# Performance work log

Measured on AMD Instinct MI355X. Metric: run time of the kernel, lower is better.

Reference implementation:

```python
import jax, jax.numpy as jnp
import numpy as np

HIDDEN = 1024
NUM_HEADS = 16
HEAD_DIM = HIDDEN // NUM_HEADS
WINDOW = 64
B, S = 2, 4096


def setup_inputs() -> dict:
    key = jax.random.key(0)
    ks = jax.random.split(key, 8)
    d = {
        'query': jax.random.normal(ks[0], (B, S, HIDDEN), jnp.float32),
        'key':   jax.random.normal(ks[1], (B, S, HIDDEN), jnp.float32),
        'value': jax.random.normal(ks[2], (B, S, HIDDEN), jnp.float32),
        'Wq': jax.random.normal(ks[3], (HIDDEN, HIDDEN), jnp.float32) * 0.02,
        'bq': jnp.zeros((HIDDEN,), jnp.float32),
        'Wk': jax.random.normal(ks[4], (HIDDEN, HIDDEN), jnp.float32) * 0.02,
        'bk': jnp.zeros((HIDDEN,), jnp.float32),
        'Wv': jax.random.normal(ks[5], (HIDDEN, HIDDEN), jnp.float32) * 0.02,
        'bv': jnp.zeros((HIDDEN,), jnp.float32),
        'Wo': jax.random.normal(ks[6], (HIDDEN, HIDDEN), jnp.float32) * 0.02,
        'bo': jnp.zeros((HIDDEN,), jnp.float32),
    }
    return d


def reference(query, key, value, Wq, bq, Wk, bk, Wv, bv, Wo, bo):
    b, s, _ = query.shape
    h, d, w = NUM_HEADS, HEAD_DIM, WINDOW
    nw = s // w
    scale = d ** -0.5
    # projections (torch Linear: x @ W.T + b)
    q = (query @ Wq.T + bq).reshape(b, s, h, d).transpose(0, 2, 1, 3)  # [b,h,s,d]
    k = (key   @ Wk.T + bk).reshape(b, s, h, d).transpose(0, 2, 1, 3)
    v = (value @ Wv.T + bv).reshape(b, s, h, d).transpose(0, 2, 1, 3)
    # split into non-overlapping windows: [b,h,nw,w,d]
    qw = q.reshape(b, h, nw, w, d)
    kw = k.reshape(b, h, nw, w, d)
    vw = v.reshape(b, h, nw, w, d)
    scores = jnp.einsum('bhnqd,bhnkd->bhnqk', qw, kw) * scale  # [b,h,nw,w,w]
    weights = jax.nn.softmax(scores, axis=-1)
    attended = jnp.einsum('bhnqk,bhnkd->bhnqd', weights, vw)   # [b,h,nw,w,d]
    attended = attended.reshape(b, h, s, d).transpose(0, 2, 1, 3).reshape(b, s, h * d)
    output = attended @ Wo.T + bo
    # block-diagonal attention map, averaged over heads -> [b,s,s]
    mean_w = weights.mean(axis=1)  # [b,nw,w,w]
    full = jnp.zeros((b, nw, w, nw, w), weights.dtype)
    idx = jnp.arange(nw)
    full = full.at[:, idx, :, idx, :].set(mean_w.transpose(1, 0, 2, 3))
    attn = full.reshape(b, s, s)
    return output, attn
```

## Files before the change

kernel.cpp:

```cpp
#include <hip/hip_runtime.h>

typedef unsigned short u16;
typedef unsigned int u32;
typedef __attribute__((ext_vector_type(8))) short bf16x8;
typedef __attribute__((ext_vector_type(4))) float f32x4;
typedef __attribute__((ext_vector_type(4))) u16 u16x4;

typedef __attribute__((address_space(1))) unsigned int as1_u32;
typedef __attribute__((address_space(3))) unsigned int as3_u32;

#define SEQ 4096
#define HID 1024
#define NHEAD 16
#define BATCH 2

__device__ __forceinline__ u16 f2b(float f) {
  union { float f; u32 u; } v; v.f = f;
  u32 r = v.u + 0x7FFFu + ((v.u >> 16) & 1u);
  return (u16)(r >> 16);
}

__device__ __forceinline__ float b2f(u16 b) {
  union { u32 u; float f; } v; v.u = ((u32)b) << 16;
  return v.f;
}

__device__ __forceinline__ void async_cp16(const void* g, void* l) {
  __builtin_amdgcn_global_load_lds((const as1_u32*)g, (as3_u32*)l, 16, 0, 0);
}

__global__ __launch_bounds__(256) void cvt_all(
    const float* __restrict__ q, const float* __restrict__ k, const float* __restrict__ v,
    const float* __restrict__ Wq, const float* __restrict__ Wk,
    const float* __restrict__ Wv, const float* __restrict__ Wo,
    u16* __restrict__ xq, u16* __restrict__ xk, u16* __restrict__ xv,
    u16* __restrict__ wq, u16* __restrict__ wk, u16* __restrict__ wv, u16* __restrict__ wo) {
  const int total = (3 << 21) + (4 << 18);
  for (int i = blockIdx.x * blockDim.x + threadIdx.x; i < total; i += gridDim.x * blockDim.x) {
    const float* src; u16* dst; int j;
    if (i < (3 << 21)) {
      const int sel = i >> 21; j = i & ((1 << 21) - 1);
      src = sel == 0 ? q : (sel == 1 ? k : v);
      dst = sel == 0 ? xq : (sel == 1 ? xk : xv);
    } else {
      const int ii = i - (3 << 21);
      const int sel = ii >> 18; j = ii & ((1 << 18) - 1);
      src = sel == 0 ? Wq : (sel == 1 ? Wk : (sel == 2 ? Wv : Wo));
      dst = sel == 0 ? wq : (sel == 1 ? wk : (sel == 2 ? wv : wo));
    }
    float4 f = ((const float4*)src)[j];
    u16x4 o; o.x = f2b(f.x); o.y = f2b(f.y); o.z = f2b(f.z); o.w = f2b(f.w);
    ((u16x4*)dst)[j] = o;
  }
}

template <int MODE>
__device__ __forceinline__ void gemm_core(
    const u16* __restrict__ A, const u16* __restrict__ Bw,
    const float* __restrict__ bias, void* __restrict__ Cout,
    u16* As, u16* Bs, long brow, long bcol) {
  const int K = HID, N = HID;
  const int tid = threadIdx.x;
  const int lane = tid & 63;
  const int wave = tid >> 6;
  const int l15 = lane & 15;
  const int quad = lane >> 4;
  const int wr = wave >> 1;
  const int wc = wave & 1;

  const int srow = lane >> 2;
  const int scol = (lane & 3) * 8;

  const u16* Ag[4]; const u16* Bg[4]; u16* Al[4]; u16* Bl[4];
#pragma unroll
  for (int j = 0; j < 4; ++j) {
    const int sub = j & 1, pan = j >> 1;
    const long roff = (wave + 4 * sub) * 16 + srow;
    const long coff = pan * 32 + scol;
    Ag[j] = A + (brow + roff) * (long)K + coff;
    Bg[j] = Bw + (bcol + roff) * (long)K + coff;
    Al[j] = As + pan * 4096 + (wave + 4 * sub) * 512;
    Bl[j] = Bs + pan * 4096 + (wave + 4 * sub) * 512;
  }

  f32x4 acc[4][4];
#pragma unroll
  for (int i = 0; i < 4; ++i)
#pragma unroll
    for (int j = 0; j < 4; ++j) acc[i][j] = f32x4{0.f, 0.f, 0.f, 0.f};

  const u16* Afb = As + (wr * 64 + l15) * 32 + quad * 8;
  const u16* Bfb = Bs + (wc * 64 + l15) * 32 + quad * 8;

  for (int k0 = 0; k0 < K; k0 += 64) {
#pragma unroll
    for (int j = 0; j < 4; ++j) {
      async_cp16(Ag[j] + k0, Al[j]);
      async_cp16(Bg[j] + k0, Bl[j]);
    }
    __syncthreads();
#pragma unroll
    for (int kh = 0; kh < 2; ++kh) {
      bf16x8 af[4], bfv[4];
#pragma unroll
      for (int mt = 0; mt < 4; ++mt) af[mt] = *(const bf16x8*)(Afb + kh * 4096 + mt * 512);
#pragma unroll
      for (int nt = 0; nt < 4; ++nt) bfv[nt] = *(const bf16x8*)(Bfb + kh * 4096 + nt * 512);
#pragma unroll
      for (int mt = 0; mt < 4; ++mt)
#pragma unroll
        for (int nt = 0; nt < 4; ++nt) {
          if (MODE == 2)
            acc[mt][nt] = __builtin_amdgcn_mfma_f32_16x16x32_bf16(af[mt], bfv[nt], acc[mt][nt], 0, 0, 0);
          else
            acc[mt][nt] = __builtin_amdgcn_mfma_f32_16x16x32_bf16(bfv[nt], af[mt], acc[mt][nt], 0, 0, 0);
        }
    }
    __syncthreads();
  }

  const long crow0 = brow + wr * 64;
  const long ccol0 = bcol + wc * 64;

  if (MODE == 2) {
#pragma unroll
    for (int nt = 0; nt < 4; ++nt) {
      const long col = ccol0 + nt * 16 + l15;
      const float bv = bias[col];
#pragma unroll
      for (int mt = 0; mt < 4; ++mt) {
        const long tokbase = crow0 + mt * 16 + quad * 4;
        const long b = tokbase >> 12;
        const long tok = tokbase & 4095;
        u16x4 pk;
        pk.x = f2b(acc[mt][nt][0] + bv);
        pk.y = f2b(acc[mt][nt][1] + bv);
        pk.z = f2b(acc[mt][nt][2] + bv);
        pk.w = f2b(acc[mt][nt][3] + bv);
        *(u16x4*)((u16*)Cout + (b * 1024 + col) * (long)SEQ + tok) = pk;
      }
    }
  } else {
#pragma unroll
    for (int nt = 0; nt < 4; ++nt) {
      const long colb = ccol0 + nt * 16 + quad * 4;
      const float4 b4 = *(const float4*)(bias + colb);
#pragma unroll
      for (int mt = 0; mt < 4; ++mt) {
        const long row = crow0 + mt * 16 + l15;
        if (MODE == 1) {
          float4 v;
          v.x = acc[mt][nt][0] + b4.x;
          v.y = acc[mt][nt][1] + b4.y;
          v.z = acc[mt][nt][2] + b4.z;
          v.w = acc[mt][nt][3] + b4.w;
          *(float4*)((float*)Cout + row * (long)N + colb) = v;
        } else {
          u16x4 pk;
          pk.x = f2b(acc[mt][nt][0] + b4.x);
          pk.y = f2b(acc[mt][nt][1] + b4.y);
          pk.z = f2b(acc[mt][nt][2] + b4.z);
          pk.w = f2b(acc[mt][nt][3] + b4.w);
          *(u16x4*)((u16*)Cout + row * (long)N + colb) = pk;
        }
      }
    }
  }
}

struct Gemm3Args {
  const u16* A[3]; const u16* W[3]; const float* bias[3]; void* C[3]; int mode[3];
};

__global__ __launch_bounds__(256, 2) void gemm_bt_fused(Gemm3Args ga) {
  __shared__ __align__(16) u16 As[2 * 128 * 32];
  __shared__ __align__(16) u16 Bs[2 * 128 * 32];
  const int z = blockIdx.z;
  const long brow = (long)blockIdx.y * 128;
  const long bcol = (long)blockIdx.x * 128;
  if (ga.mode[z] == 2)
    gemm_core<2>(ga.A[z], ga.W[z], ga.bias[z], ga.C[z], As, Bs, brow, bcol);
  else
    gemm_core<0>(ga.A[z], ga.W[z], ga.bias[z], ga.C[z], As, Bs, brow, bcol);
}

__global__ __launch_bounds__(256, 4) void attn_win(
    const u16* __restrict__ qp, const u16* __restrict__ kp,
    const u16* __restrict__ vT, u16* __restrict__ attended,
    float* __restrict__ Psum) {
  __shared__ __align__(16) u16 Plds[4][32][72];

  const int tid = threadIdx.x;
  const int lane = tid & 63;
  const int wave = tid >> 6;
  const int l15 = lane & 15;
  const int quad = lane >> 4;

  const int idx = blockIdx.x;
  const int half = idx & 1;
  const int hg = (idx >> 1) & 3;
  const int wn = idx >> 3;
  const int b = wn >> 6;
  const int n = wn & 63;
  const int h = hg * 4 + wave;

  const long qrow0 = (long)b * SEQ + (long)n * 64 + half * 32;
  const long krow0 = (long)b * SEQ + (long)n * 64;
  const long cbase = (long)h * 64;

  u16(*Pw)[72] = Plds[wave];

  f32x4 s[2][4];
#pragma unroll
  for (int i = 0; i < 2; ++i)
#pragma unroll
    for (int j = 0; j < 4; ++j) s[i][j] = f32x4{0.f, 0.f, 0.f, 0.f};
#pragma unroll
  for (int kt = 0; kt < 2; ++kt) {
    bf16x8 aq[2], bkf[4];
#pragma unroll
    for (int mt = 0; mt < 2; ++mt)
      aq[mt] = *(const bf16x8*)(qp + (qrow0 + mt * 16 + l15) * HID + cbase + kt * 32 + quad * 8);
#pragma unroll
    for (int nt = 0; nt < 4; ++nt)
      bkf[nt] = *(const bf16x8*)(kp + (krow0 + nt * 16 + l15) * HID + cbase + kt * 32 + quad * 8);
#pragma unroll
    for (int mt = 0; mt < 2; ++mt)
#pragma unroll
      for (int nt = 0; nt < 4; ++nt)
        s[mt][nt] = __builtin_amdgcn_mfma_f32_16x16x32_bf16(bkf[nt], aq[mt], s[mt][nt], 0, 0, 0);
  }

#pragma unroll
  for (int mt = 0; mt < 2; ++mt) {
    float m = -1e30f;
#pragma unroll
    for (int nt = 0; nt < 4; ++nt)
#pragma unroll
      for (int r = 0; r < 4; ++r) { s[mt][nt][r] *= 0.125f; m = fmaxf(m, s[mt][nt][r]); }
    m = fmaxf(m, __shfl_xor(m, 16));
    m = fmaxf(m, __shfl_xor(m, 32));
    float sum = 0.f;
#pragma unroll
    for (int nt = 0; nt < 4; ++nt)
#pragma unroll
      for (int r = 0; r < 4; ++r) { float e = __expf(s[mt][nt][r] - m); s[mt][nt][r] = e; sum += e; }
    sum += __shfl_xor(sum, 16);
    sum += __shfl_xor(sum, 32);
    const float inv = 1.f / sum;
#pragma unroll
    for (int nt = 0; nt < 4; ++nt)
#pragma unroll
      for (int r = 0; r < 4; ++r) s[mt][nt][r] *= inv;
  }

#pragma unroll
  for (int mt = 0; mt < 2; ++mt)
#pragma unroll
    for (int nt = 0; nt < 4; ++nt) {
      u16x4 pk;
      pk.x = f2b(s[mt][nt][0]);
      pk.y = f2b(s[mt][nt][1]);
      pk.z = f2b(s[mt][nt][2]);
      pk.w = f2b(s[mt][nt][3]);
      *(u16x4*)(&Pw[mt * 16 + l15][nt * 16 + quad * 4]) = pk;
    }

  f32x4 o[2][4];
#pragma unroll
  for (int i = 0; i < 2; ++i)
#pragma unroll
    for (int j = 0; j < 4; ++j) o[i][j] = f32x4{0.f, 0.f, 0.f, 0.f};
  const long vbase = ((long)(b * 16 + h) * 64) * SEQ;
#pragma unroll
  for (int kt = 0; kt < 2; ++kt) {
    bf16x8 ap[2], bvf[4];
#pragma unroll
    for (int mt = 0; mt < 2; ++mt)
      ap[mt] = *(const bf16x8*)(&Pw[mt * 16 + l15][kt * 32 + quad * 8]);
#pragma unroll
    for (int nt = 0; nt < 4; ++nt)
      bvf[nt] = *(const bf16x8*)(vT + vbase + (long)(nt * 16 + l15) * SEQ + n * 64 + kt * 32 + quad * 8);
#pragma unroll
    for (int mt = 0; mt < 2; ++mt)
#pragma unroll
      for (int nt = 0; nt < 4; ++nt)
        o[mt][nt] = __builtin_amdgcn_mfma_f32_16x16x32_bf16(bvf[nt], ap[mt], o[mt][nt], 0, 0, 0);
  }

#pragma unroll
  for (int mt = 0; mt < 2; ++mt)
#pragma unroll
    for (int nt = 0; nt < 4; ++nt) {
      const long row = qrow0 + mt * 16 + l15;
      const long col = cbase + nt * 16 + quad * 4;
      u16x4 pk;
      pk.x = f2b(o[mt][nt][0]);
      pk.y = f2b(o[mt][nt][1]);
      pk.z = f2b(o[mt][nt][2]);
      pk.w = f2b(o[mt][nt][3]);
      *(u16x4*)(attended + row * HID + col) = pk;
    }

  __syncthreads();
  float* pbase = Psum + (long)idx * 2048;
  for (int i = tid; i < 32 * 64; i += 256) {
    const int r = i >> 6, c = i & 63;
    float sacc = 0.f;
#pragma unroll
    for (int w = 0; w < 4; ++w) sacc += b2f(Plds[w][r][c]);
    pbase[i] = sacc;
  }
}

__global__ __launch_bounds__(256, 2) void gemm_o_expand(
    const u16* __restrict__ A, const u16* __restrict__ Bw,
    const float* __restrict__ bias, float* __restrict__ Cout,
    const float* __restrict__ Psum, float* __restrict__ attn) {
  __shared__ __align__(16) u16 As[2 * 128 * 32];
  __shared__ __align__(16) u16 Bs[2 * 128 * 32];

  const int tid = threadIdx.x;

  if (blockIdx.x >= 512) {
    const long e = blockIdx.x - 512;
    const long f0 = e * 4096;
#pragma unroll
    for (int it = 0; it < 16; ++it) {
      const long f = f0 + it * 256 + tid;
      const int b = (int)(f >> 22);
      const int rem = (int)(f & ((1 << 22) - 1));
      const int row = rem >> 10;
      const int c4 = rem & 1023;
      const int n = row >> 6;
      float4 val = {0.f, 0.f, 0.f, 0.f};
      const int d4 = c4 - n * 16;
      if ((unsigned)d4 < 16u) {
        const int r = row & 63;
        const int half = r >> 5, rr = r & 31;
        const long base = ((long)((b * 64 + n) * 8 + half)) * 2048 + rr * 64 + d4 * 4;
        float4 p0 = *(const float4*)(Psum + base);
        float4 p1 = *(const float4*)(Psum + base + 4096);
        float4 p2 = *(const float4*)(Psum + base + 8192);
        float4 p3 = *(const float4*)(Psum + base + 12288);
        val.x = (p0.x + p1.x + p2.x + p3.x) * (1.f / 16.f);
        val.y = (p0.y + p1.y + p2.y + p3.y) * (1.f / 16.f);
        val.z = (p0.z + p1.z + p2.z + p3.z) * (1.f / 16.f);
        val.w = (p0.w + p1.w + p2.w + p3.w) * (1.f / 16.f);
      }
      ((float4*)attn)[f] = val;
    }
    return;
  }

  const long brow = (long)(blockIdx.x >> 3) * 128;
  const long bcol = (long)(blockIdx.x & 7) * 128;
  gemm_core<1>(A, Bw, bias, Cout, As, Bs, brow, bcol);
}

extern "C" void kernel_launch(void* const* d_in, const int* in_sizes, int n_in,
                              void* d_out, int out_size, void* d_ws, size_t ws_size,
                              hipStream_t stream) {
  (void)in_sizes; (void)n_in; (void)out_size; (void)ws_size;
  const float* query = (const float*)d_in[0];
  const float* key   = (const float*)d_in[1];
  const float* value = (const float*)d_in[2];
  const float* Wq = (const float*)d_in[3];
  const float* bq = (const float*)d_in[4];
  const float* Wk = (const float*)d_in[5];
  const float* bk = (const float*)d_in[6];
  const float* Wv = (const float*)d_in[7];
  const float* bv = (const float*)d_in[8];
  const float* Wo = (const float*)d_in[9];
  const float* bo = (const float*)d_in[10];

  float* out  = (float*)d_out;
  float* attn = out + (size_t)BATCH * SEQ * HID;

  char* ws = (char*)d_ws;
  const size_t MB = (size_t)1 << 20;
  u16* xq = (u16*)(ws + 0 * MB);
  u16* xk = (u16*)(ws + 16 * MB);
  u16* xv = (u16*)(ws + 32 * MB);
  u16* wq = (u16*)(ws + 48 * MB);
  u16* wk = (u16*)(ws + 50 * MB);
  u16* wv = (u16*)(ws + 52 * MB);
  u16* wo = (u16*)(ws + 54 * MB);
  u16* qp = (u16*)(ws + 56 * MB);
  u16* kp = (u16*)(ws + 72 * MB);
  u16* vT = (u16*)(ws + 88 * MB);
  float* Psum = (float*)(ws + 104 * MB);
  u16* att = xq;

  cvt_all<<<3584, 256, 0, stream>>>(query, key, value, Wq, Wk, Wv, Wo,
                                    xq, xk, xv, wq, wk, wv, wo);

  Gemm3Args ga;
  ga.A[0] = xq; ga.W[0] = wq; ga.bias[0] = bq; ga.C[0] = qp; ga.mode[0] = 0;
  ga.A[1] = xk; ga.W[1] = wk; ga.bias[1] = bk; ga.C[1] = kp; ga.mode[1] = 0;
  ga.A[2] = xv; ga.W[2] = wv; ga.bias[2] = bv; ga.C[2] = vT; ga.mode[2] = 2;
  dim3 g3(HID / 128, (BATCH * SEQ) / 128, 3);
  gemm_bt_fused<<<g3, 256, 0, stream>>>(ga);

  attn_win<<<BATCH * 64 * 4 * 2, 256, 0, stream>>>(qp, kp, vT, att, Psum);

  gemm_o_expand<<<512 + 2048, 256, 0, stream>>>(att, wo, bo, out, Psum, attn);
}
```

Measured before the change: 391.9 us.

## Zero attention map during QKV GEMM and write only diagonal blocks later

Zero-filling the 128MB attention map moves into an extra z-slice of the fused QKV projection launch, so it can overlap the GEMM tiles. The output-projection kernel now launches only 128 extra blocks, and each writes just one 64x64 diagonal block averaged over the four partial sums. This removes the full-matrix pass with per-element index math from the final kernel. The zeroing blocks now compete with the GEMM for bandwidth and CU slots in the first launch.

```diff
diff --git a/kernel.cpp b/kernel.cpp
--- a/kernel.cpp
+++ b/kernel.cpp
@@ -172,10 +172,21 @@
   const u16* A[3]; const u16* W[3]; const float* bias[3]; void* C[3]; int mode[3];
 };
 
-__global__ __launch_bounds__(256, 2) void gemm_bt_fused(Gemm3Args ga) {
+__global__ __launch_bounds__(256, 2) void gemm_bt_fused(Gemm3Args ga, float* __restrict__ attn) {
   __shared__ __align__(16) u16 As[2 * 128 * 32];
   __shared__ __align__(16) u16 Bs[2 * 128 * 32];
   const int z = blockIdx.z;
+  const int tid = threadIdx.x;
+
+  if (z == 3) {
+    const long e = (long)blockIdx.y * 8 + blockIdx.x;
+    float4* dst = (float4*)attn + e * 16384;
+#pragma unroll
+    for (int it = 0; it < 64; ++it)
+      dst[it * 256 + tid] = float4{0.f, 0.f, 0.f, 0.f};
+    return;
+  }
+
   const long brow = (long)blockIdx.y * 128;
   const long bcol = (long)blockIdx.x * 128;
   if (ga.mode[z] == 2)
@@ -323,32 +334,26 @@
   const int tid = threadIdx.x;
 
   if (blockIdx.x >= 512) {
-    const long e = blockIdx.x - 512;
-    const long f0 = e * 4096;
-#pragma unroll
-    for (int it = 0; it < 16; ++it) {
-      const long f = f0 + it * 256 + tid;
-      const int b = (int)(f >> 22);
-      const int rem = (int)(f & ((1 << 22) - 1));
-      const int row = rem >> 10;
-      const int c4 = rem & 1023;
-      const int n = row >> 6;
-      float4 val = {0.f, 0.f, 0.f, 0.f};
-      const int d4 = c4 - n * 16;
-      if ((unsigned)d4 < 16u) {
-        const int r = row & 63;
-        const int half = r >> 5, rr = r & 31;
-        const long base = ((long)((b * 64 + n) * 8 + half)) * 2048 + rr * 64 + d4 * 4;
-        float4 p0 = *(const float4*)(Psum + base);
-        float4 p1 = *(const float4*)(Psum + base + 4096);
-        float4 p2 = *(const float4*)(Psum + base + 8192);
-        float4 p3 = *(const float4*)(Psum + base + 12288);
-        val.x = (p0.x + p1.x + p2.x + p3.x) * (1.f / 16.f);
-        val.y = (p0.y + p1.y + p2.y + p3.y) * (1.f / 16.f);
-        val.z = (p0.z + p1.z + p2.z + p3.z) * (1.f / 16.f);
-        val.w = (p0.w + p1.w + p2.w + p3.w) * (1.f / 16.f);
-      }
-      ((float4*)attn)[f] = val;
+    const int e = blockIdx.x - 512;
+    const int b = e >> 6, n = e & 63;
+    float* obase = attn + (long)b * SEQ * SEQ + (long)n * 64 * SEQ + (long)n * 64;
+    const long pb = (long)((b * 64 + n) * 8) * 2048;
+#pragma unroll
+    for (int it = 0; it < 4; ++it) {
+      const int li = it * 256 + tid;
+      const int r = li >> 4, c4 = li & 15;
+      const int half = r >> 5, rr = r & 31;
+      const long base = pb + half * 2048 + rr * 64 + c4 * 4;
+      float4 p0 = *(const float4*)(Psum + base);
+      float4 p1 = *(const float4*)(Psum + base + 4096);
+      float4 p2 = *(const float4*)(Psum + base + 8192);
+      float4 p3 = *(const float4*)(Psum + base + 12288);
+      float4 val;
+      val.x = (p0.x + p1.x + p2.x + p3.x) * (1.f / 16.f);
+      val.y = (p0.y + p1.y + p2.y + p3.y) * (1.f / 16.f);
+      val.z = (p0.z + p1.z + p2.z + p3.z) * (1.f / 16.f);
+      val.w = (p0.w + p1.w + p2.w + p3.w) * (1.f / 16.f);
+      *(float4*)(obase + (long)r * SEQ + c4 * 4) = val;
     }
     return;
   }
@@ -399,10 +404,10 @@
   ga.A[0] = xq; ga.W[0] = wq; ga.bias[0] = bq; ga.C[0] = qp; ga.mode[0] = 0;
   ga.A[1] = xk; ga.W[1] = wk; ga.bias[1] = bk; ga.C[1] = kp; ga.mode[1] = 0;
   ga.A[2] = xv; ga.W[2] = wv; ga.bias[2] = bv; ga.C[2] = vT; ga.mode[2] = 2;
-  dim3 g3(HID / 128, (BATCH * SEQ) / 128, 3);
-  gemm_bt_fused<<<g3, 256, 0, stream>>>(ga);
+  dim3 g4(HID / 128, (BATCH * SEQ) / 128, 4);
+  gemm_bt_fused<<<g4, 256, 0, stream>>>(ga, attn);
 
   attn_win<<<BATCH * 64 * 4 * 2, 256, 0, stream>>>(qp, kp, vT, att, Psum);
 
-  gemm_o_expand<<<512 + 2048, 256, 0, stream>>>(att, wo, bo, out, Psum, attn);
-}
+  gemm_o_expand<<<512 + 128, 256, 0, stream>>>(att, wo, bo, out, Psum, attn);
+}
```

Result: no change. 390.9 us (-0.2%).
